# Kernel optimization log

Hardware: AMD Instinct MI355X
Metric: run time of the kernel (lower is better)

The kernel has to match this reference:

```python
import jax, jax.numpy as jnp
import numpy as np

B, S, D = 2, 2048, 256
N_QK, N_V = 8192, 8192
NCPS = 32            # n_cells_per_side
MPC = 16             # max entries per cell -> 9*MPC = 144 candidates
MAX_K_QK, MAX_K_V = 32, 64
POS_MIN = jnp.array([-4.0, -4.0], dtype=jnp.float32)
POS_RANGE = jnp.array([8.0, 8.0], dtype=jnp.float32)
_OFF = jnp.array([[-1, -1], [-1, 0], [-1, 1], [0, -1], [0, 0], [0, 1], [1, -1], [1, 0], [1, 1]], dtype=jnp.int32)


def cell_lookup(query_pos, cell_map):
    # query_pos: [B,S,2], cell_map: [NCPS*NCPS, MPC] int32, -1 = padding
    Bq, Sq, _ = query_pos.shape
    mpc = cell_map.shape[1]
    normalized = (query_pos - POS_MIN) / POS_RANGE
    cell_xy = jnp.clip((normalized * NCPS).astype(jnp.int32), 0, NCPS - 1)
    nbr = jnp.clip(cell_xy[:, :, None, :] + _OFF[None, None, :, :], 0, NCPS - 1)  # [B,S,9,2]
    nbr_idx = nbr[..., 0] * NCPS + nbr[..., 1]                                     # [B,S,9]
    cand = cell_map[nbr_idx].reshape(Bq, Sq, 9 * mpc)
    valid = cand >= 0
    return jnp.where(valid, cand, 0), valid


def threshold_gate(scores, tau, max_k):
    raw = scores - tau
    gate = jnp.where(raw > 0, raw, 1e-8 * jnp.exp(raw))
    exp_gate = jnp.exp(gate) - 1.0
    k = min(max_k, scores.shape[-1])
    topv, _ = jax.lax.top_k(exp_gate, k)
    thr = topv[:, :, -1:]
    exp_gate = jnp.where(exp_gate >= thr, exp_gate, 0.0)
    gate_sum = exp_gate.sum(axis=-1, keepdims=True) + 1e-8
    strength = jnp.tanh(exp_gate.max(axis=-1, keepdims=True))
    return exp_gate / gate_sum * strength


def setup_inputs() -> dict:
    key = jax.random.key(0)
    ks = jax.random.split(key, 11)
    x = jax.random.normal(ks[0], (B, S, D), jnp.float32)
    qk_neurons = jax.random.normal(ks[1], (N_QK, D), jnp.float32) * 0.02
    v_neurons = jax.random.normal(ks[2], (N_V, D), jnp.float32) * 0.02
    neuron_pos = jax.random.normal(ks[3], (N_QK + N_V, 2), jnp.float32)
    W_pos_qk = jax.random.normal(ks[4], (D, 2), jnp.float32) * 0.05
    b_pos_qk = jnp.zeros((2,), jnp.float32)
    W_pos_v = jax.random.normal(ks[5], (D, 2), jnp.float32) * 0.05
    b_pos_v = jnp.zeros((2,), jnp.float32)
    W_tau = jax.random.normal(ks[6], (D, 3), jnp.float32) * 0.02
    b_tau = jnp.zeros((3,), jnp.float32)
    cm_qk = jax.random.randint(ks[7], (NCPS * NCPS, MPC), 0, N_QK)
    cm_qk = jnp.where(jax.random.bernoulli(ks[8], 0.15, cm_qk.shape), -1, cm_qk).astype(jnp.int32)
    cm_v = jax.random.randint(ks[9], (NCPS * NCPS, MPC), 0, N_V)
    cm_v = jnp.where(jax.random.bernoulli(ks[10], 0.15, cm_v.shape), -1, cm_v).astype(jnp.int32)
    return {"x": x, "qk_neurons": qk_neurons, "v_neurons": v_neurons, "neuron_pos": neuron_pos,
            "W_pos_qk": W_pos_qk, "b_pos_qk": b_pos_qk, "W_pos_v": W_pos_v, "b_pos_v": b_pos_v,
            "W_tau": W_tau, "b_tau": b_tau, "cell_map_qk": cm_qk, "cell_map_v": cm_v}


def reference(x, qk_neurons, v_neurons, neuron_pos, W_pos_qk, b_pos_qk, W_pos_v, b_pos_v, W_tau, b_tau, cell_map_qk, cell_map_v):
    qk_pos = x @ W_pos_qk + b_pos_qk        # [B,S,2]
    v_pos = x @ W_pos_v + b_pos_v
    ci_qk, m_qk = cell_lookup(qk_pos, cell_map_qk)   # [B,S,144]
    ci_v, m_v = cell_lookup(v_pos, cell_map_v)
    cand_qk = qk_neurons[ci_qk]             # [B,S,144,D] gather (dominant traffic)
    cand_v = v_neurons[ci_v]
    # dropout is deterministic (eval) -> identity; scores_Q == scores_K in source
    s_qk = jnp.where(m_qk, jnp.einsum('bsd,bsnd->bsn', x, cand_qk), -1e9)
    s_v = jnp.where(m_v, jnp.einsum('bsd,bsnd->bsn', x, cand_v), -1e9)
    tau = x @ W_tau + b_tau                 # [B,S,3]
    gQ = threshold_gate(s_qk, tau[:, :, 0:1], MAX_K_QK)
    gK = threshold_gate(s_qk, tau[:, :, 1:2], MAX_K_QK)
    gV = threshold_gate(s_v, tau[:, :, 2:3], MAX_K_V)
    npos_qk = neuron_pos[:N_QK]
    npos_v = neuron_pos[N_QK:N_QK + N_V]
    d_qk = jnp.sum((qk_pos[:, :, None, :] - npos_qk[ci_qk]) ** 2, axis=-1)
    d_v = jnp.sum((v_pos[:, :, None, :] - npos_v[ci_v]) ** 2, axis=-1)
    pos_loss = (jax.lax.stop_gradient(gQ) * d_qk * m_qk).sum() / (m_qk.sum() + 1e-8) \
             + (jax.lax.stop_gradient(gV) * d_v * m_v).sum() / (m_v.sum() + 1e-8)
    return jnp.stack([gQ, gK, gV]), pos_loss
```

## Files before the change

kernel.cpp:

```cpp
#include <hip/hip_runtime.h>
#include <math.h>

#define BB 2
#define SS 2048
#define DD 256
#define NTOK (BB * SS)
#define N_QK 8192
#define N_V  8192
#define NCPS 32
#define MPC  16
#define NC   144
#define K_QK 32
#define K_V  64
#define OUT_GATES (3 * NTOK * NC)

__device__ __forceinline__ float blockSum(float v, volatile float* red) {
    for (int o = 32; o; o >>= 1) v += __shfl_down(v, o, 64);
    int lane = threadIdx.x & 63, wid = threadIdx.x >> 6;
    __syncthreads();
    if (lane == 0) red[wid] = v;
    __syncthreads();
    return red[0] + red[1] + red[2] + red[3];
}

__device__ __forceinline__ float blockMin(float v, volatile float* red) {
    for (int o = 32; o; o >>= 1) v = fminf(v, __shfl_down(v, o, 64));
    int lane = threadIdx.x & 63, wid = threadIdx.x >> 6;
    __syncthreads();
    if (lane == 0) red[wid] = v;
    __syncthreads();
    return fminf(fminf(red[0], red[1]), fminf(red[2], red[3]));
}

__device__ __forceinline__ float blockMax(float v, volatile float* red) {
    for (int o = 32; o; o >>= 1) v = fmaxf(v, __shfl_down(v, o, 64));
    int lane = threadIdx.x & 63, wid = threadIdx.x >> 6;
    __syncthreads();
    if (lane == 0) red[wid] = v;
    __syncthreads();
    return fmaxf(fmaxf(red[0], red[1]), fmaxf(red[2], red[3]));
}

__global__ __launch_bounds__(256) void router_main(
    const float* __restrict__ x,
    const float* __restrict__ qk_neurons,
    const float* __restrict__ v_neurons,
    const float* __restrict__ neuron_pos,
    const float* __restrict__ W_pos_qk, const float* __restrict__ b_pos_qk,
    const float* __restrict__ W_pos_v,  const float* __restrict__ b_pos_v,
    const float* __restrict__ W_tau,    const float* __restrict__ b_tau,
    const int* __restrict__ cm_qk, const int* __restrict__ cm_v,
    float* __restrict__ out, float* __restrict__ ws)
{
    const int token = blockIdx.x;
    const int tid   = threadIdx.x;
    const int lane  = tid & 63, wid = tid >> 6;

    __shared__ float  x_s[DD];
    __shared__ float  scal[8];
    __shared__ double partd[4][7];
    __shared__ int    ci_s[2][NC];
    __shared__ float  sc_s[2][NC];
    __shared__ float  d_s[2][NC];
    __shared__ float  eg_s[NC];
    __shared__ float  red[4];

    float xv = x[(size_t)token * DD + tid];
    x_s[tid] = xv;
    double p[7];
    p[0] = (double)xv * (double)W_pos_qk[tid * 2 + 0];
    p[1] = (double)xv * (double)W_pos_qk[tid * 2 + 1];
    p[2] = (double)xv * (double)W_pos_v[tid * 2 + 0];
    p[3] = (double)xv * (double)W_pos_v[tid * 2 + 1];
    p[4] = (double)xv * (double)W_tau[tid * 3 + 0];
    p[5] = (double)xv * (double)W_tau[tid * 3 + 1];
    p[6] = (double)xv * (double)W_tau[tid * 3 + 2];
    #pragma unroll
    for (int j = 0; j < 7; ++j) {
        double v = p[j];
        for (int o = 32; o; o >>= 1) v += __shfl_down(v, o, 64);
        p[j] = v;
    }
    if (lane == 0) {
        #pragma unroll
        for (int j = 0; j < 7; ++j) partd[wid][j] = p[j];
    }
    __syncthreads();
    if (tid < 7) {
        double v = partd[0][tid] + partd[1][tid] + partd[2][tid] + partd[3][tid];
        float bias = (tid < 2) ? b_pos_qk[tid]
                   : (tid < 4) ? b_pos_v[tid - 2]
                               : b_tau[tid - 4];
        scal[tid] = (float)v + bias;
    }
    __syncthreads();

    for (int c = tid; c < 2 * NC; c += 256) {
        int side = (c >= NC);
        int n    = side ? c - NC : c;
        float px = scal[side * 2 + 0], py = scal[side * 2 + 1];
        int cx = (int)(((px + 4.0f) / 8.0f) * 32.0f);
        int cy = (int)(((py + 4.0f) / 8.0f) * 32.0f);
        cx = min(max(cx, 0), NCPS - 1);
        cy = min(max(cy, 0), NCPS - 1);
        int o = n / MPC, slot = n % MPC;
        int nx = min(max(cx + (o / 3 - 1), 0), NCPS - 1);
        int ny = min(max(cy + (o % 3 - 1), 0), NCPS - 1);
        int idx = nx * NCPS + ny;
        int cand = (side ? cm_v : cm_qk)[idx * MPC + slot];
        ci_s[side][n] = cand;
        const float* npos = neuron_pos + (side ? (size_t)N_QK * 2 : 0);
        int cidx = max(cand, 0);
        float dx = px - npos[cidx * 2 + 0];
        float dy = py - npos[cidx * 2 + 1];
        d_s[side][n] = dx * dx + dy * dy;
    }
    __syncthreads();

    {
        const int quad = tid >> 2, ql = tid & 3;
        const float4* x4 = (const float4*)x_s;
        for (int c = quad; c < 2 * NC; c += 64) {
            int side = (c >= NC);
            int n    = side ? c - NC : c;
            int cand = ci_s[side][n];
            const float4* row = (const float4*)((side ? v_neurons : qk_neurons)
                                                + (size_t)max(cand, 0) * DD);
            double acc = 0.0;
            #pragma unroll
            for (int i = ql; i < 64; i += 4) {
                float4 r  = row[i];
                float4 xx = x4[i];
                acc += (double)r.x * (double)xx.x + (double)r.y * (double)xx.y
                     + (double)r.z * (double)xx.z + (double)r.w * (double)xx.w;
            }
            acc += __shfl_xor(acc, 1, 64);
            acc += __shfl_xor(acc, 2, 64);
            if (ql == 0)
                sc_s[side][n] = (cand >= 0) ? (float)acc : -1e9f;
        }
    }
    __syncthreads();

    #pragma unroll 1
    for (int g = 0; g < 3; ++g) {
        const int side = (g == 2);
        const int k    = (g == 2) ? K_V : K_QK;
        const float tau = scal[4 + g];

        if (tid < NC) {
            float s   = sc_s[side][tid];
            float raw = s - tau;
            float gate = (raw > 0.0f) ? raw : 1e-8f * expf(raw);
            eg_s[tid] = expf(gate) - 1.0f;
        }
        __syncthreads();

        float myeg = (tid < NC) ? eg_s[tid] : 0.0f;
        float thr_cand = 3.402823466e38f;
        if (tid < NC) {
            int cnt = 0;
            for (int j = 0; j < NC; ++j) cnt += (eg_s[j] > myeg) ? 1 : 0;
            if (cnt < k) thr_cand = myeg;
        }
        float thr = blockMin(thr_cand, red);

        float keep = (tid < NC && myeg >= thr) ? myeg : 0.0f;
        float gs   = blockSum(keep, red) + 1e-8f;
        float mx   = blockMax(myeg, red);
        float strength = tanhf(mx);
        float outv = keep / gs * strength;

        if (tid < NC)
            out[((size_t)g * NTOK + token) * NC + tid] = outv;

        if (g == 0 || g == 2) {
            float m = (tid < NC && ci_s[side][tid] >= 0) ? 1.0f : 0.0f;
            float contrib = outv * d_s[side][tid < NC ? tid : 0] * m;
            float wsum = blockSum(contrib, red);
            float csum = blockSum(m, red);
            if (tid == 0) {
                ws[(size_t)token * 4 + (g ? 2 : 0)] = wsum;
                ws[(size_t)token * 4 + (g ? 3 : 1)] = csum;
            }
        }
        __syncthreads();
    }
}

__global__ void router_finalize(const float* __restrict__ ws, float* __restrict__ out) {
    const int t = threadIdx.x;
    double wq = 0, cq = 0, wv = 0, cv = 0;
    for (int i = t; i < NTOK; i += 64) {
        wq += (double)ws[(size_t)i * 4 + 0];
        cq += (double)ws[(size_t)i * 4 + 1];
        wv += (double)ws[(size_t)i * 4 + 2];
        cv += (double)ws[(size_t)i * 4 + 3];
    }
    for (int o = 32; o; o >>= 1) {
        wq += __shfl_down(wq, o, 64);
        cq += __shfl_down(cq, o, 64);
        wv += __shfl_down(wv, o, 64);
        cv += __shfl_down(cv, o, 64);
    }
    if (t == 0)
        out[OUT_GATES] = (float)(wq / (cq + 1e-8) + wv / (cv + 1e-8));
}

extern "C" void kernel_launch(void* const* d_in, const int* in_sizes, int n_in,
                              void* d_out, int out_size, void* d_ws, size_t ws_size,
                              hipStream_t stream) {
    const float* x          = (const float*)d_in[0];
    const float* qk_neurons = (const float*)d_in[1];
    const float* v_neurons  = (const float*)d_in[2];
    const float* neuron_pos = (const float*)d_in[3];
    const float* W_pos_qk   = (const float*)d_in[4];
    const float* b_pos_qk   = (const float*)d_in[5];
    const float* W_pos_v    = (const float*)d_in[6];
    const float* b_pos_v    = (const float*)d_in[7];
    const float* W_tau      = (const float*)d_in[8];
    const float* b_tau      = (const float*)d_in[9];
    const int*   cm_qk      = (const int*)d_in[10];
    const int*   cm_v       = (const int*)d_in[11];

    float* out = (float*)d_out;
    float* ws  = (float*)d_ws;

    router_main<<<NTOK, 256, 0, stream>>>(
        x, qk_neurons, v_neurons, neuron_pos,
        W_pos_qk, b_pos_qk, W_pos_v, b_pos_v, W_tau, b_tau,
        cm_qk, cm_v, out, ws);
    router_finalize<<<1, 64, 0, stream>>>(ws, out);
}
```

Measured before the change: 215.9 us.

## Process all three gates concurrently with wave-level reductions and widen finalize

The gating phase no longer loops over the three gates with repeated block-wide barrier reductions. It now computes all exp-gates and top-k rank counts in parallel across the block, then assigns one wavefront per gate for the min/max/sum reductions using only shuffles. The double-precision dot product uses four independent FMA accumulators to shorten the dependency chain. The finalize kernel grows from 64 to 1024 threads with float4 loads. The cost is a slightly different summation order, but it stays in double precision.

```diff
diff --git a/kernel.cpp b/kernel.cpp
--- a/kernel.cpp
+++ b/kernel.cpp
@@ -13,33 +13,6 @@
 #define K_QK 32
 #define K_V  64
 #define OUT_GATES (3 * NTOK * NC)
-
-__device__ __forceinline__ float blockSum(float v, volatile float* red) {
-    for (int o = 32; o; o >>= 1) v += __shfl_down(v, o, 64);
-    int lane = threadIdx.x & 63, wid = threadIdx.x >> 6;
-    __syncthreads();
-    if (lane == 0) red[wid] = v;
-    __syncthreads();
-    return red[0] + red[1] + red[2] + red[3];
-}
-
-__device__ __forceinline__ float blockMin(float v, volatile float* red) {
-    for (int o = 32; o; o >>= 1) v = fminf(v, __shfl_down(v, o, 64));
-    int lane = threadIdx.x & 63, wid = threadIdx.x >> 6;
-    __syncthreads();
-    if (lane == 0) red[wid] = v;
-    __syncthreads();
-    return fminf(fminf(red[0], red[1]), fminf(red[2], red[3]));
-}
-
-__device__ __forceinline__ float blockMax(float v, volatile float* red) {
-    for (int o = 32; o; o >>= 1) v = fmaxf(v, __shfl_down(v, o, 64));
-    int lane = threadIdx.x & 63, wid = threadIdx.x >> 6;
-    __syncthreads();
-    if (lane == 0) red[wid] = v;
-    __syncthreads();
-    return fmaxf(fmaxf(red[0], red[1]), fmaxf(red[2], red[3]));
-}
 
 __global__ __launch_bounds__(256) void router_main(
     const float* __restrict__ x,
@@ -56,14 +29,14 @@
     const int tid   = threadIdx.x;
     const int lane  = tid & 63, wid = tid >> 6;
 
-    __shared__ float  x_s[DD];
+    __shared__ __align__(16) float  x_s[DD];
     __shared__ float  scal[8];
     __shared__ double partd[4][7];
     __shared__ int    ci_s[2][NC];
     __shared__ float  sc_s[2][NC];
     __shared__ float  d_s[2][NC];
-    __shared__ float  eg_s[NC];
-    __shared__ float  red[4];
+    __shared__ __align__(16) float eg3[3][NC];
+    __shared__ float  tc3[3][NC];
 
     float xv = x[(size_t)token * DD + tid];
     x_s[tid] = xv;
@@ -126,14 +99,17 @@
             int cand = ci_s[side][n];
             const float4* row = (const float4*)((side ? v_neurons : qk_neurons)
                                                 + (size_t)max(cand, 0) * DD);
-            double acc = 0.0;
+            double ax = 0.0, ay = 0.0, az = 0.0, aw = 0.0;
             #pragma unroll
             for (int i = ql; i < 64; i += 4) {
                 float4 r  = row[i];
                 float4 xx = x4[i];
-                acc += (double)r.x * (double)xx.x + (double)r.y * (double)xx.y
-                     + (double)r.z * (double)xx.z + (double)r.w * (double)xx.w;
+                ax = fma((double)r.x, (double)xx.x, ax);
+                ay = fma((double)r.y, (double)xx.y, ay);
+                az = fma((double)r.z, (double)xx.z, az);
+                aw = fma((double)r.w, (double)xx.w, aw);
             }
+            double acc = (ax + ay) + (az + aw);
             acc += __shfl_xor(acc, 1, 64);
             acc += __shfl_xor(acc, 2, 64);
             if (ql == 0)
@@ -142,60 +118,94 @@
     }
     __syncthreads();
 
-    #pragma unroll 1
-    for (int g = 0; g < 3; ++g) {
-        const int side = (g == 2);
-        const int k    = (g == 2) ? K_V : K_QK;
-        const float tau = scal[4 + g];
-
-        if (tid < NC) {
-            float s   = sc_s[side][tid];
-            float raw = s - tau;
-            float gate = (raw > 0.0f) ? raw : 1e-8f * expf(raw);
-            eg_s[tid] = expf(gate) - 1.0f;
-        }
-        __syncthreads();
-
-        float myeg = (tid < NC) ? eg_s[tid] : 0.0f;
-        float thr_cand = 3.402823466e38f;
-        if (tid < NC) {
-            int cnt = 0;
-            for (int j = 0; j < NC; ++j) cnt += (eg_s[j] > myeg) ? 1 : 0;
-            if (cnt < k) thr_cand = myeg;
-        }
-        float thr = blockMin(thr_cand, red);
-
-        float keep = (tid < NC && myeg >= thr) ? myeg : 0.0f;
-        float gs   = blockSum(keep, red) + 1e-8f;
-        float mx   = blockMax(myeg, red);
-        float strength = tanhf(mx);
-        float outv = keep / gs * strength;
-
-        if (tid < NC)
-            out[((size_t)g * NTOK + token) * NC + tid] = outv;
-
-        if (g == 0 || g == 2) {
-            float m = (tid < NC && ci_s[side][tid] >= 0) ? 1.0f : 0.0f;
-            float contrib = outv * d_s[side][tid < NC ? tid : 0] * m;
-            float wsum = blockSum(contrib, red);
-            float csum = blockSum(m, red);
-            if (tid == 0) {
-                ws[(size_t)token * 4 + (g ? 2 : 0)] = wsum;
-                ws[(size_t)token * 4 + (g ? 3 : 1)] = csum;
+    for (int idx = tid; idx < 3 * NC; idx += 256) {
+        int g = (idx >= 2 * NC) ? 2 : (idx >= NC ? 1 : 0);
+        int j = idx - g * NC;
+        float s   = sc_s[g == 2][j];
+        float raw = s - scal[4 + g];
+        float gate = (raw > 0.0f) ? raw : 1e-8f * expf(raw);
+        eg3[g][j] = expf(gate) - 1.0f;
+    }
+    __syncthreads();
+
+    for (int idx = tid; idx < 3 * NC; idx += 256) {
+        int g = (idx >= 2 * NC) ? 2 : (idx >= NC ? 1 : 0);
+        int j = idx - g * NC;
+        float my = eg3[g][j];
+        const float4* e4 = (const float4*)&eg3[g][0];
+        int cnt = 0;
+        #pragma unroll
+        for (int q = 0; q < NC / 4; ++q) {
+            float4 e = e4[q];
+            cnt += (e.x > my) + (e.y > my) + (e.z > my) + (e.w > my);
+        }
+        int k = (g == 2) ? K_V : K_QK;
+        tc3[g][j] = (cnt < k) ? my : 3.402823466e38f;
+    }
+    __syncthreads();
+
+    if (wid < 3) {
+        const int g = wid, side = (g == 2);
+        const bool has2 = (lane < 16);
+        float e0 = eg3[g][lane],       e1 = eg3[g][lane + 64];
+        float t0 = tc3[g][lane],       t1 = tc3[g][lane + 64];
+        float e2 = has2 ? eg3[g][lane + 128] : 0.0f;
+        float t2 = has2 ? tc3[g][lane + 128] : 3.402823466e38f;
+        float mn = fminf(fminf(t0, t1), t2);
+        float mx = fmaxf(fmaxf(e0, e1), e2);
+        #pragma unroll
+        for (int o = 32; o; o >>= 1) {
+            mn = fminf(mn, __shfl_xor(mn, o, 64));
+            mx = fmaxf(mx, __shfl_xor(mx, o, 64));
+        }
+        const float thr = mn;
+        float k0 = (e0 >= thr) ? e0 : 0.0f;
+        float k1 = (e1 >= thr) ? e1 : 0.0f;
+        float k2 = (has2 && e2 >= thr) ? e2 : 0.0f;
+        float sum = k0 + k1 + k2;
+        #pragma unroll
+        for (int o = 32; o; o >>= 1) sum += __shfl_xor(sum, o, 64);
+        const float gs = sum + 1e-8f;
+        const float strength = tanhf(mx);
+        float o0 = k0 / gs * strength;
+        float o1 = k1 / gs * strength;
+        float o2 = k2 / gs * strength;
+        float* og = out + ((size_t)g * NTOK + token) * NC;
+        og[lane]      = o0;
+        og[lane + 64] = o1;
+        if (has2) og[lane + 128] = o2;
+
+        if (g != 1) {
+            float m0 = (ci_s[side][lane]       >= 0) ? 1.0f : 0.0f;
+            float m1 = (ci_s[side][lane + 64]  >= 0) ? 1.0f : 0.0f;
+            float m2 = (has2 && ci_s[side][lane + 128] >= 0) ? 1.0f : 0.0f;
+            float w = o0 * d_s[side][lane] * m0 + o1 * d_s[side][lane + 64] * m1;
+            if (has2) w += o2 * d_s[side][lane + 128] * m2;
+            float c = m0 + m1 + m2;
+            #pragma unroll
+            for (int o = 32; o; o >>= 1) {
+                w += __shfl_xor(w, o, 64);
+                c += __shfl_xor(c, o, 64);
             }
-        }
-        __syncthreads();
+            if (lane == 0) {
+                ws[(size_t)token * 4 + (side ? 2 : 0)] = w;
+                ws[(size_t)token * 4 + (side ? 3 : 1)] = c;
+            }
+        }
     }
 }
 
-__global__ void router_finalize(const float* __restrict__ ws, float* __restrict__ out) {
-    const int t = threadIdx.x;
+__global__ __launch_bounds__(1024) void router_finalize(
+    const float* __restrict__ ws, float* __restrict__ out)
+{
+    __shared__ double red[16][4];
+    const int t = threadIdx.x, lane = t & 63, w = t >> 6;
     double wq = 0, cq = 0, wv = 0, cv = 0;
-    for (int i = t; i < NTOK; i += 64) {
-        wq += (double)ws[(size_t)i * 4 + 0];
-        cq += (double)ws[(size_t)i * 4 + 1];
-        wv += (double)ws[(size_t)i * 4 + 2];
-        cv += (double)ws[(size_t)i * 4 + 3];
+    const float4* w4 = (const float4*)ws;
+    for (int i = t; i < NTOK; i += 1024) {
+        float4 v = w4[i];
+        wq += (double)v.x; cq += (double)v.y;
+        wv += (double)v.z; cv += (double)v.w;
     }
     for (int o = 32; o; o >>= 1) {
         wq += __shfl_down(wq, o, 64);
@@ -203,8 +213,15 @@
         wv += __shfl_down(wv, o, 64);
         cv += __shfl_down(cv, o, 64);
     }
-    if (t == 0)
-        out[OUT_GATES] = (float)(wq / (cq + 1e-8) + wv / (cv + 1e-8));
+    if (lane == 0) { red[w][0] = wq; red[w][1] = cq; red[w][2] = wv; red[w][3] = cv; }
+    __syncthreads();
+    if (t == 0) {
+        double a = 0, b = 0, c = 0, d = 0;
+        for (int i = 0; i < 16; ++i) {
+            a += red[i][0]; b += red[i][1]; c += red[i][2]; d += red[i][3];
+        }
+        out[OUT_GATES] = (float)(a / (b + 1e-8) + c / (d + 1e-8));
+    }
 }
 
 extern "C" void kernel_launch(void* const* d_in, const int* in_sizes, int n_in,
@@ -230,5 +247,5 @@
         x, qk_neurons, v_neurons, neuron_pos,
         W_pos_qk, b_pos_qk, W_pos_v, b_pos_v, W_tau, b_tau,
         cm_qk, cm_v, out, ws);
-    router_finalize<<<1, 64, 0, stream>>>(ws, out);
+    router_finalize<<<1, 1024, 0, stream>>>(ws, out);
 }
```

Measured after the change: 199.1 us. 1.08x faster.
